# Optimization experiments

Measured on AMD Instinct MI355X. Metric: run time of the kernel, lower is better.

## Reference

```python
import jax, jax.numpy as jnp
import numpy as np
import math

H, D, DEG = 8, 64, 2
GATE_BIAS = 6.906768

def _rope(x, sin, cos):
    # GPT-J style interleaved rotary: even lanes = x1*cos - x2*sin, odd = x2*cos + x1*sin
    x1, x2 = x[..., ::2], x[..., 1::2]
    s = sin[None, :, None, :]
    c = cos[None, :, None, :]
    even = x1 * c - x2 * s
    odd = x2 * c + x1 * s
    return jnp.stack([even, odd], axis=-1).reshape(x.shape)

def _forward(x, w_attn, w_proj):
    B, T, C = x.shape
    h, d, deg = H, D, DEG
    hd = h * d
    scale = 1.0 / math.sqrt(d)
    qkvg = x @ w_attn                                   # (B,T,3hd+h)
    q = qkvg[..., :hd].reshape(B, T, h, d)
    k = qkvg[..., hd:2 * hd].reshape(B, T, h, d)
    v = qkvg[..., 2 * hd:3 * hd].reshape(B, T, h, d)
    log_g = jax.nn.log_sigmoid(GATE_BIAS + qkvg[..., 3 * hd:].astype(jnp.float32))  # (B,T,h)
    # sinusoidal RoPE with frequency 2*pi / T**(2i/d), as in get_sinusoidal_embeddings
    pos = jnp.arange(T, dtype=jnp.float32)
    div = 2.0 * math.pi / (float(T) ** (jnp.arange(0, d, 2, dtype=jnp.float32) / d))
    ang = pos[:, None] * div[None, :]                   # (T, d//2)
    sin, cos = jnp.sin(ang), jnp.cos(ang)
    q = _rope(q, sin, cos)
    k = _rope(k, sin, cos)
    # gated symmetric-power attention: quadratic reference of chunked power_full
    # score_ts = (scale * q_t . k_s)^deg * exp(L_t - L_s), causal, row-normalized
    L = jnp.cumsum(log_g, axis=1).transpose(0, 2, 1)    # (B,h,T) cumulative log-gates
    qk = jnp.einsum('bthd,bshd->bhts', q, k) * scale    # (B,h,T,T)
    log_gate = L[:, :, :, None] - L[:, :, None, :]      # L_t - L_s
    causal = jnp.tril(jnp.ones((T, T), dtype=bool))
    scores = jnp.where(causal, (qk ** deg) * jnp.exp(log_gate), 0.0)
    denom = jnp.maximum(scores.sum(-1, keepdims=True), 1e-6)
    y = jnp.einsum('bhts,bshd->bthd', scores / denom, v)  # (B,T,h,d)
    return y.reshape(B, T, hd) @ w_proj

def setup_inputs() -> dict:
    key = jax.random.key(0)
    k1, k2, k3 = jax.random.split(key, 3)
    B, T, C = 2, 2048, 512
    x = jax.random.normal(k1, (B, T, C), dtype=jnp.float32)
    w_attn = jax.random.normal(k2, (C, 3 * H * D + H), dtype=jnp.float32) * 0.02
    w_proj = jax.random.normal(k3, (H * D, C), dtype=jnp.float32) * 0.02
    return {"x": x, "w_attn": w_attn, "w_proj": w_proj}

def reference(x, w_attn, w_proj):
    return _forward(x, w_attn, w_proj)
```

## Files before the change

### kernel.cpp

```cpp
#include <hip/hip_runtime.h>
#include <hip/hip_bf16.h>
#include <math.h>

constexpr int B_ = 2, T_ = 2048, C_ = 512, H_ = 8, D_ = 64;
constexpr int QKVG_ = 3 * H_ * D_ + H_;
constexpr float GATE_BIAS_ = 6.906768f;
constexpr int N1_ = 1536;
constexpr int SC_ = 8;
constexpr int NBLK_ = 1280;
constexpr int MC_ = 4096 * 512;
constexpr int BHT_ = B_ * H_ * T_;

typedef __attribute__((ext_vector_type(8))) short short8;
typedef __attribute__((ext_vector_type(4))) float f32x4;

__device__ __forceinline__ unsigned short f2b(float f) {
    union { __hip_bfloat16 h; unsigned short u; } cv;
    cv.h = __float2bfloat16(f);
    return cv.u;
}
__device__ __forceinline__ short8 pack8(float4 a, float4 b) {
    short8 r;
    r[0] = (short)f2b(a.x); r[1] = (short)f2b(a.y);
    r[2] = (short)f2b(a.z); r[3] = (short)f2b(a.w);
    r[4] = (short)f2b(b.x); r[5] = (short)f2b(b.y);
    r[6] = (short)f2b(b.z); r[7] = (short)f2b(b.w);
    return r;
}

__device__ __forceinline__ void gl2lds16(const unsigned short* g, void* lds_base) {
    __builtin_amdgcn_global_load_lds(
        (const __attribute__((address_space(1))) unsigned int*)g,
        (__attribute__((address_space(3))) unsigned int*)lds_base, 16, 0, 0);
}

__device__ __forceinline__ void packT_body(
    const float* __restrict__ W, unsigned short* __restrict__ Bt,
    int K, int N, int ldW, int nt, int kt, int tid, float (*Ws)[65])
{
    {
        const int r = tid >> 2;
        const int c0 = (tid & 3) * 16;
#pragma unroll
        for (int j = 0; j < 16; ++j) {
            const int n = nt + c0 + j;
            Ws[r][c0 + j] = (n < N) ? W[(size_t)(kt + r) * ldW + n] : 0.f;
        }
    }
    __syncthreads();
    {
        const int d = tid >> 2;
        const int cc = tid & 3;
        const int kc = cc * 16;
        short8 o0, o1;
#pragma unroll
        for (int j = 0; j < 8; ++j) o0[j] = (short)f2b(Ws[kc + j][d]);
#pragma unroll
        for (int j = 0; j < 8; ++j) o1[j] = (short)f2b(Ws[kc + 8 + j][d]);
        const int row = nt + d;
        unsigned short* op = Bt + (size_t)row * K + kt;
        *(short8*)(op + ((2 * cc) ^ (row & 7)) * 8)     = o0;
        *(short8*)(op + ((2 * cc + 1) ^ (row & 7)) * 8) = o1;
    }
}

__global__ __launch_bounds__(256) void pack_inputs(
    const float* __restrict__ x, const float* __restrict__ w_attn,
    const float* __restrict__ w_proj, unsigned short* __restrict__ xb,
    unsigned short* __restrict__ Bt1, unsigned short* __restrict__ Bt2,
    float2* __restrict__ sincos, float* __restrict__ g)
{
    __shared__ float SM[64 * 65];
    float (*Ws)[65] = (float(*)[65])SM;
    const int bid = blockIdx.x;
    const int tid = threadIdx.x;
    if (bid < 1024) {
        const int i = bid * 256 + tid;
        float4 f0 = *(const float4*)(x + (size_t)i * 8);
        float4 f1 = *(const float4*)(x + (size_t)i * 8 + 4);
        const int row = i >> 6;
        const int ic = i & 63;
        const int swc = (ic & ~7) | ((ic & 7) ^ (row & 7));
        *(short8*)(xb + (size_t)row * 512 + swc * 8) = pack8(f0, f1);
    } else if (bid < 1216) {
        const int q = bid - 1024;
        packT_body(w_attn, Bt1, C_, N1_, QKVG_, (q % 24) * 64, (q / 24) * 64, tid, Ws);
    } else if (bid < 1280) {
        const int q = bid - 1216;
        packT_body(w_proj, Bt2, H_ * D_, C_, C_, (q & 7) * 64, (q >> 3) * 64, tid, Ws);
    } else if (bid < 1288) {
        const int t = (bid - 1280) * 256 + tid;
        float2* op = sincos + (size_t)t * 32;
#pragma unroll
        for (int i = 0; i < 32; ++i) {
            const float div = 6.2831853071795864f * exp2f((float)i * (-11.0f / 32.0f));
            const float ang = (float)t * div;
            op[i] = make_float2(cosf(ang), sinf(ang));
        }
    } else {
        const int q = bid - 1288;
        float* LDSw = SM;
        {
            const int k = tid * 2;
#pragma unroll
            for (int kk = 0; kk < 2; ++kk) {
                const float* wp = w_attn + (size_t)(k + kk) * QKVG_ + 1536;
                float4 wa = *(const float4*)wp;
                float4 wb = *(const float4*)(wp + 4);
                float* dst = LDSw + (k + kk) * 8;
                *(float4*)dst = wa;
                *(float4*)(dst + 4) = wb;
            }
        }
        __syncthreads();
        const int m = q * 32 + (tid >> 3);
        const int h = tid & 7;
        const float* xrow = x + (size_t)m * C_;
        float s = 0.f;
#pragma unroll 4
        for (int k0 = 0; k0 < 512; k0 += 4) {
            float4 xv = *(const float4*)(xrow + k0);
            s += xv.x * LDSw[(k0 + 0) * 8 + h] + xv.y * LDSw[(k0 + 1) * 8 + h]
               + xv.z * LDSw[(k0 + 2) * 8 + h] + xv.w * LDSw[(k0 + 3) * 8 + h];
        }
        const int b = m >> 11, t = m & 2047;
        g[(size_t)(b * 8 + h) * T_ + t] = s;
    }
}

__global__ __launch_bounds__(256) void gate_cumsum(
    const float* __restrict__ g, float* __restrict__ Lg)
{
    __shared__ float wsum[4];
    const int bh = blockIdx.x;
    const int tid = threadIdx.x;
    const int lane = tid & 63, wv = tid >> 6;

    const float* gp = g + (size_t)bh * T_ + tid * 8;
    float v[8];
    float s = 0.f;
#pragma unroll
    for (int j = 0; j < 8; ++j) {
        const float z = gp[j] + GATE_BIAS_;
        const float lg = (z > 0.f) ? -log1pf(expf(-z)) : (z - log1pf(expf(z)));
        s += lg;
        v[j] = s;
    }
    float ssum = s;
#pragma unroll
    for (int off = 1; off < 64; off <<= 1) {
        float n = __shfl_up(ssum, off, 64);
        if (lane >= off) ssum += n;
    }
    if (lane == 63) wsum[wv] = ssum;
    __syncthreads();
    float base = ssum - s;
#pragma unroll
    for (int w = 0; w < 3; ++w)
        base += (w < wv) ? wsum[w] : 0.f;

    float* op = Lg + (size_t)bh * T_ + tid * 8;
#pragma unroll
    for (int j = 0; j < 8; ++j) op[j] = v[j] + base;
}

__global__ __launch_bounds__(256) void gemm_fused(
    const unsigned short* __restrict__ A, const unsigned short* __restrict__ Bt,
    const float* __restrict__ Lg, const float2* __restrict__ sincos,
    unsigned short* __restrict__ Qsb, unsigned short* __restrict__ Ksb,
    unsigned short* __restrict__ Vtb)
{
    __shared__ __align__(16) char smem[65536];
    float (*epi)[65] = (float(*)[65])smem;

    const int tid = threadIdx.x;
    const int wave = tid >> 6, lane = tid & 63;
    const int l15 = lane & 15, lhi = lane >> 4;
    const int wr = wave >> 1, wc = wave & 1;
    const int bm = blockIdx.y * 128, bn = blockIdx.x * 128;

    f32x4 acc[4][4];
#pragma unroll
    for (int i = 0; i < 4; ++i)
#pragma unroll
        for (int j = 0; j < 4; ++j) acc[i][j] = (f32x4){0.f, 0.f, 0.f, 0.f};

    const unsigned short* Arow = A + (size_t)bm * C_;
    const unsigned short* Brow = Bt + (size_t)bn * C_;
    const int sw = (l15 & 7) << 4;
    const int srow = tid >> 3;
    const int schunk = tid & 7;

#pragma unroll
    for (int p = 0; p < 4; ++p) {
        const int row = p * 32 + srow;
        const size_t goff = (size_t)row * C_ + schunk * 8;
        gl2lds16(Arow + goff, smem + p * 4096 + wave * 1024);
        gl2lds16(Brow + goff, smem + 16384 + p * 4096 + wave * 1024);
    }

    for (int ks = 0; ks < 8; ++ks) {
        __syncthreads();
        if (ks < 7) {
            char* dst = smem + ((ks + 1) & 1) * 32768;
            const int k1 = (ks + 1) * 64;
#pragma unroll
            for (int p = 0; p < 4; ++p) {
                const int row = p * 32 + srow;
                const size_t goff = (size_t)row * C_ + k1 + schunk * 8;
                gl2lds16(Arow + goff, dst + p * 4096 + wave * 1024);
                gl2lds16(Brow + goff, dst + 16384 + p * 4096 + wave * 1024);
            }
        }
        const char* AsB = smem + (ks & 1) * 32768;
        const char* BsB = AsB + 16384;

        short8 af[4][2];
#pragma unroll
        for (int mi = 0; mi < 4; ++mi) {
            const int row = wr * 64 + mi * 16 + l15;
#pragma unroll
            for (int kk = 0; kk < 2; ++kk)
                af[mi][kk] = *(const short8*)(AsB + row * 128 + ((kk * 64 + lhi * 16) ^ sw));
        }
#pragma unroll
        for (int ni = 0; ni < 4; ++ni) {
            const int row = wc * 64 + ni * 16 + l15;
            short8 bf0 = *(const short8*)(BsB + row * 128 + ((lhi * 16) ^ sw));
            short8 bf1 = *(const short8*)(BsB + row * 128 + ((64 + lhi * 16) ^ sw));
#pragma unroll
            for (int mi = 0; mi < 4; ++mi) {
                acc[mi][ni] = __builtin_amdgcn_mfma_f32_16x16x32_bf16(af[mi][0], bf0, acc[mi][ni], 0, 0, 0);
                acc[mi][ni] = __builtin_amdgcn_mfma_f32_16x16x32_bf16(af[mi][1], bf1, acc[mi][ni], 0, 0, 0);
            }
        }
    }

    const int rid = bn >> 9;
    const int b = bm >> 11;
    const int tloc0 = bm & 2047;

#pragma unroll
    for (int hc = 0; hc < 2; ++hc) {
        __syncthreads();
        if (wc == hc) {
#pragma unroll
            for (int mi = 0; mi < 4; ++mi)
#pragma unroll
                for (int ni = 0; ni < 4; ++ni)
#pragma unroll
                    for (int r = 0; r < 4; ++r)
                        epi[wr * 64 + mi * 16 + lhi * 4 + r][ni * 16 + l15] = acc[mi][ni][r];
        }
        __syncthreads();
        const int h = ((bn & 511) >> 6) + hc;
        const int bh = b * 8 + h;
        if (rid < 2) {
            const int row = tid >> 1;
            const int c0 = (tid & 1) * 32;
            const int t = tloc0 + row;
            const float Lt = Lg[(size_t)bh * T_ + t];
            const float scl = (rid == 0) ? (__expf(0.5f * Lt) * 0.125f)
                                         : __expf(-0.5f * Lt);
            float vb[32];
#pragma unroll
            for (int j = 0; j < 32; ++j) vb[j] = epi[row][c0 + j];
            const float2* sct = sincos + (size_t)t * 32 + (c0 >> 1);
#pragma unroll
            for (int p = 0; p < 16; ++p) {
                const float2 cssn = sct[p];
                const float x1 = vb[2 * p], x2 = vb[2 * p + 1];
                vb[2 * p]     = (x1 * cssn.x - x2 * cssn.y) * scl;
                vb[2 * p + 1] = (x2 * cssn.x + x1 * cssn.y) * scl;
            }
            unsigned short* op = ((rid == 0) ? Qsb : Ksb) + ((size_t)bh * T_ + t) * 64;
#pragma unroll
            for (int j = 0; j < 4; ++j) {
                short8 o = pack8(*(float4*)&vb[j * 8], *(float4*)&vb[j * 8 + 4]);
                const int chunk = (c0 >> 3) + j;
                const int pos = (rid == 0) ? chunk : (chunk ^ (t & 7));
                *(short8*)(op + pos * 8) = o;
            }
        } else {
            const int d = tid >> 2;
            const int tq = tid & 3;
            unsigned short* op = Vtb + ((size_t)(bh * 64 + d)) * T_;
#pragma unroll
            for (int j = 0; j < 4; ++j) {
                const int tl = tq * 32 + j * 8;
                short8 o;
#pragma unroll
                for (int e = 0; e < 8; ++e)
                    o[e] = (short)f2b(epi[tl + e][d]);
                const int chunkidx = (tloc0 + tl) >> 3;
                const int pos = (chunkidx & ~7) | ((chunkidx & 7) ^ (d & 7));
                *(short8*)(op + pos * 8) = o;
            }
        }
    }
}

__global__ __launch_bounds__(256) void gemm_bf16(
    const unsigned short* __restrict__ A, const unsigned short* __restrict__ Bt,
    float* __restrict__ C, int M, int N, int K)
{
    __shared__ __align__(16) char smem[49152];

    const int tid = threadIdx.x;
    const int wave = tid >> 6, lane = tid & 63;
    const int l15 = lane & 15, lhi = lane >> 4;
    const int wr = wave >> 1, wc = wave & 1;
    const int bm = blockIdx.y * 64, bn = blockIdx.x * 128;

    f32x4 acc[2][4];
#pragma unroll
    for (int i = 0; i < 2; ++i)
#pragma unroll
        for (int j = 0; j < 4; ++j) acc[i][j] = (f32x4){0.f, 0.f, 0.f, 0.f};

    const unsigned short* Arow = A + (size_t)bm * K;
    const unsigned short* Brow = Bt + (size_t)bn * K;
    const int sw = (l15 & 7) << 4;
    const int srow = tid >> 3;
    const int schunk = tid & 7;
    const int nks = K >> 6;

#pragma unroll
    for (int p = 0; p < 2; ++p) {
        const int row = p * 32 + srow;
        gl2lds16(Arow + (size_t)row * K + schunk * 8, smem + p * 4096 + wave * 1024);
    }
#pragma unroll
    for (int p = 0; p < 4; ++p) {
        const int row = p * 32 + srow;
        gl2lds16(Brow + (size_t)row * K + schunk * 8, smem + 8192 + p * 4096 + wave * 1024);
    }

    for (int ks = 0; ks < nks; ++ks) {
        __syncthreads();
        if (ks + 1 < nks) {
            char* dst = smem + ((ks + 1) & 1) * 24576;
            const int k1 = (ks + 1) * 64;
#pragma unroll
            for (int p = 0; p < 2; ++p) {
                const int row = p * 32 + srow;
                gl2lds16(Arow + (size_t)row * K + k1 + schunk * 8, dst + p * 4096 + wave * 1024);
            }
#pragma unroll
            for (int p = 0; p < 4; ++p) {
                const int row = p * 32 + srow;
                gl2lds16(Brow + (size_t)row * K + k1 + schunk * 8, dst + 8192 + p * 4096 + wave * 1024);
            }
        }
        const char* AsB = smem + (ks & 1) * 24576;
        const char* BsB = AsB + 8192;

        short8 af[2][2];
#pragma unroll
        for (int mi = 0; mi < 2; ++mi) {
            const int row = wr * 32 + mi * 16 + l15;
#pragma unroll
            for (int kk = 0; kk < 2; ++kk)
                af[mi][kk] = *(const short8*)(AsB + row * 128 + ((kk * 64 + lhi * 16) ^ sw));
        }
#pragma unroll
        for (int ni = 0; ni < 4; ++ni) {
            const int row = wc * 64 + ni * 16 + l15;
            short8 bf0 = *(const short8*)(BsB + row * 128 + ((lhi * 16) ^ sw));
            short8 bf1 = *(const short8*)(BsB + row * 128 + ((64 + lhi * 16) ^ sw));
#pragma unroll
            for (int mi = 0; mi < 2; ++mi) {
                acc[mi][ni] = __builtin_amdgcn_mfma_f32_16x16x32_bf16(af[mi][0], bf0, acc[mi][ni], 0, 0, 0);
                acc[mi][ni] = __builtin_amdgcn_mfma_f32_16x16x32_bf16(af[mi][1], bf1, acc[mi][ni], 0, 0, 0);
            }
        }
    }

#pragma unroll
    for (int mi = 0; mi < 2; ++mi) {
        const int gm = bm + wr * 32 + mi * 16 + lhi * 4;
#pragma unroll
        for (int r = 0; r < 4; ++r) {
            float* crow = C + (size_t)(gm + r) * N;
#pragma unroll
            for (int ni = 0; ni < 4; ++ni) {
                const int gn = bn + wc * 64 + ni * 16 + l15;
                if (gn < N) crow[gn] = acc[mi][ni][r];
            }
        }
    }
}

__global__ __launch_bounds__(256) void attn_mfma(
    const unsigned short* __restrict__ Qsb, const unsigned short* __restrict__ Ksb,
    const unsigned short* __restrict__ Vtb,
    float* __restrict__ Y0, float* __restrict__ Yp, float* __restrict__ Dpart)
{
    __shared__ __align__(16) char smem[40960];
    char* PsB = smem + 32768;

    const int wg = blockIdx.x;
    const int xcd = wg & 7;
    const int slot = wg >> 3;
    const int bh = (slot < 80) ? xcd : 8 + xcd;
    const int rem = (slot < 80) ? slot : slot - 80;
    const int rr = 79 - rem;
    int bt, sc;
    if (rr < 8)       { bt = rr; sc = 0; }
    else if (rr < 24) { const int q = rr - 8;  bt = 8 + (q >> 1);  sc = q & 1; }
    else if (rr < 48) { const int q = rr - 24; bt = 16 + q / 3;    sc = q % 3; }
    else              { const int q = rr - 48; bt = 24 + (q >> 2); sc = q & 3; }
    const int st0 = sc * SC_;
    const int st1 = min(st0 + SC_ - 1, bt);

    const int tid = threadIdx.x;
    const int wave = tid >> 6;
    const int lane = tid & 63;
    const int l15 = lane & 15;
    const int lhi = lane >> 4;
    const int b = bh >> 3, h = bh & 7;
    const int t0 = bt * 64;

    const int qrow = t0 + wave * 16 + l15;
    const unsigned short* qpp = Qsb + ((size_t)bh * T_ + qrow) * 64 + lhi * 8;
    short8 qf[2];
    qf[0] = *(const short8*)(qpp);
    qf[1] = *(const short8*)(qpp + 32);

    f32x4 accY[4];
#pragma unroll
    for (int n = 0; n < 4; ++n) accY[n] = (f32x4){0.f, 0.f, 0.f, 0.f};
    float den[4] = {0.f, 0.f, 0.f, 0.f};

    const int kchunk = lhi * 16;
    const int rsw = (l15 & 7) << 4;
    const int srow = tid >> 3;
    const int schunk = tid & 7;

#pragma unroll
    for (int p = 0; p < 2; ++p) {
        const int row = p * 32 + srow;
        gl2lds16(Ksb + ((size_t)bh * T_ + st0 * 64 + row) * 64 + schunk * 8,
                 smem + p * 4096 + wave * 1024);
        gl2lds16(Vtb + ((size_t)bh * 64 + row) * T_ + st0 * 64 + schunk * 8,
                 smem + 8192 + p * 4096 + wave * 1024);
    }

    for (int st = st0; st <= st1; ++st) {
        __syncthreads();
        if (st < st1) {
            char* dst = smem + (((st - st0) + 1) & 1) * 16384;
            const int s1 = (st + 1) * 64;
#pragma unroll
            for (int p = 0; p < 2; ++p) {
                const int row = p * 32 + srow;
                gl2lds16(Ksb + ((size_t)bh * T_ + s1 + row) * 64 + schunk * 8,
                         dst + p * 4096 + wave * 1024);
                gl2lds16(Vtb + ((size_t)bh * 64 + row) * T_ + s1 + schunk * 8,
                         dst + 8192 + p * 4096 + wave * 1024);
            }
        }
        const char* KsB = smem + ((st - st0) & 1) * 16384;
        const char* VtB = KsB + 8192;

        f32x4 accS[4];
#pragma unroll
        for (int n = 0; n < 4; ++n) accS[n] = (f32x4){0.f, 0.f, 0.f, 0.f};
        __builtin_amdgcn_s_setprio(1);
#pragma unroll
        for (int n = 0; n < 4; ++n) {
#pragma unroll
            for (int kk = 0; kk < 2; ++kk) {
                short8 bf = *(const short8*)(KsB + (n * 16 + l15) * 128 + ((kk * 64 + kchunk) ^ rsw));
                accS[n] = __builtin_amdgcn_mfma_f32_16x16x32_bf16(qf[kk], bf, accS[n], 0, 0, 0);
            }
        }
        __builtin_amdgcn_s_setprio(0);

        const bool last = (st == bt);
        char* PsW = PsB + wave * 2048;
#pragma unroll
        for (int n = 0; n < 4; ++n) {
#pragma unroll
            for (int r = 0; r < 4; ++r) {
                const float a = accS[n][r];
                float p = a * a;
                if (last)
                    p = ((n * 16 + l15) <= wave * 16 + lhi * 4 + r) ? p : 0.f;
                den[r] += p;
                const int prow = lhi * 4 + r;
                *(unsigned short*)(PsW + prow * 128 + ((2 * (n * 16 + l15)) ^ ((prow & 7) << 4))) = f2b(p);
            }
        }

        short8 pa[2];
#pragma unroll
        for (int kk = 0; kk < 2; ++kk)
            pa[kk] = *(const short8*)(PsW + l15 * 128 + ((kk * 64 + kchunk) ^ rsw));
        __builtin_amdgcn_s_setprio(1);
#pragma unroll
        for (int n = 0; n < 4; ++n) {
#pragma unroll
            for (int kk = 0; kk < 2; ++kk) {
                short8 vb = *(const short8*)(VtB + (n * 16 + l15) * 128 + ((kk * 64 + kchunk) ^ rsw));
                accY[n] = __builtin_amdgcn_mfma_f32_16x16x32_bf16(pa[kk], vb, accY[n], 0, 0, 0);
            }
        }
        __builtin_amdgcn_s_setprio(0);
    }

#pragma unroll
    for (int r = 0; r < 4; ++r) {
        den[r] += __shfl_xor(den[r], 1, 64);
        den[r] += __shfl_xor(den[r], 2, 64);
        den[r] += __shfl_xor(den[r], 4, 64);
        den[r] += __shfl_xor(den[r], 8, 64);
    }

    float* Ybase = (sc == 0) ? Y0 : (Yp + (size_t)(sc - 1) * MC_);
    float* Dbase = Dpart + (size_t)sc * BHT_;
#pragma unroll
    for (int r = 0; r < 4; ++r) {
        const int t = t0 + wave * 16 + lhi * 4 + r;
        if (l15 == 0)
            Dbase[(size_t)bh * T_ + t] = den[r];
        float* yo = Ybase + (size_t)(b * T_ + t) * (H_ * D_) + h * 64 + l15;
#pragma unroll
        for (int n = 0; n < 4; ++n)
            yo[n * 16] = accY[n][r];
    }
}

__global__ __launch_bounds__(256) void normalize_kernel(
    const float* __restrict__ Y0, const float* __restrict__ Yp,
    const float* __restrict__ Dpart, unsigned short* __restrict__ ybb)
{
    const int gid = blockIdx.x * 256 + threadIdx.x;
    const size_t base = (size_t)gid * 8;
    const int row = (int)(base >> 9);
    const int col = (int)(base & 511);
    const int b = row >> 11, t = row & 2047, h = col >> 6;
    const int bh = b * H_ + h;
    const int nsc = ((t >> 6) >> 3) + 1;

    float d = Dpart[(size_t)bh * T_ + t];
    float4 f0 = *(const float4*)(Y0 + base);
    float4 f1 = *(const float4*)(Y0 + base + 4);
    for (int s = 1; s < nsc; ++s) {
        d += Dpart[(size_t)s * BHT_ + (size_t)bh * T_ + t];
        const float* yp = Yp + (size_t)(s - 1) * MC_ + base;
        float4 g0 = *(const float4*)(yp);
        float4 g1 = *(const float4*)(yp + 4);
        f0.x += g0.x; f0.y += g0.y; f0.z += g0.z; f0.w += g0.w;
        f1.x += g1.x; f1.y += g1.y; f1.z += g1.z; f1.w += g1.w;
    }
    const float inv = 1.0f / fmaxf(d, 1e-6f);
    f0.x *= inv; f0.y *= inv; f0.z *= inv; f0.w *= inv;
    f1.x *= inv; f1.y *= inv; f1.z *= inv; f1.w *= inv;

    const int ic = col >> 3;
    const int swc = (ic & ~7) | ((ic & 7) ^ (row & 7));
    *(short8*)(ybb + (size_t)row * 512 + swc * 8) = pack8(f0, f1);
}

extern "C" void kernel_launch(void* const* d_in, const int* in_sizes, int n_in,
                              void* d_out, int out_size, void* d_ws, size_t ws_size,
                              hipStream_t stream)
{
    const float* x      = (const float*)d_in[0];
    const float* w_attn = (const float*)d_in[1];
    const float* w_proj = (const float*)d_in[2];
    float* out = (float*)d_out;

    char* p = (char*)d_ws;
    float2* sincos = (float2*)p;               p += (size_t)T_ * 32 * 8;
    float* g       = (float*)p;                p += (size_t)BHT_ * 4;
    float* Lg      = (float*)p;                p += (size_t)BHT_ * 4;
    float* Dpart   = (float*)p;                p += (size_t)4 * BHT_ * 4;
    unsigned short* xb  = (unsigned short*)p;  p += (size_t)MC_ * 2;
    unsigned short* Bt1 = (unsigned short*)p;  p += (size_t)N1_ * C_ * 2;
    unsigned short* Bt2 = (unsigned short*)p;  p += (size_t)C_ * C_ * 2;
    unsigned short* Qsb = (unsigned short*)p;  p += (size_t)BHT_ * 64 * 2;
    unsigned short* Ksb = (unsigned short*)p;  p += (size_t)BHT_ * 64 * 2;
    unsigned short* Vtb = (unsigned short*)p;  p += (size_t)BHT_ * 64 * 2;
    float* Yp      = (float*)p;                p += (size_t)3 * MC_ * 4;
    unsigned short* ybb = (unsigned short*)p;

    const int M = B_ * T_;

    pack_inputs<<<1416, 256, 0, stream>>>(x, w_attn, w_proj, xb, Bt1, Bt2, sincos, g);

    gate_cumsum<<<B_ * H_, 256, 0, stream>>>(g, Lg);

    gemm_fused<<<dim3(N1_ / 128, M / 128), 256, 0, stream>>>(
        xb, Bt1, Lg, sincos, Qsb, Ksb, Vtb);

    attn_mfma<<<NBLK_, 256, 0, stream>>>(Qsb, Ksb, Vtb, out, Yp, Dpart);

    normalize_kernel<<<(MC_ / 8) / 256, 256, 0, stream>>>(out, Yp, Dpart, ybb);

    gemm_bf16<<<dim3(C_ / 128, M / 64), 256, 0, stream>>>(
        ybb, Bt2, out, M, C_, H_ * D_);
}
```

Baseline: 79.15 us.

## Enlarge attention query tile to 128 rows to reuse K/V tiles across two row-tiles

```diff
diff --git a/kernel.cpp b/kernel.cpp
--- a/kernel.cpp
+++ b/kernel.cpp
@@ -6,8 +6,7 @@
 constexpr int QKVG_ = 3 * H_ * D_ + H_;
 constexpr float GATE_BIAS_ = 6.906768f;
 constexpr int N1_ = 1536;
-constexpr int SC_ = 8;
-constexpr int NBLK_ = 1280;
+constexpr int NBLK_ = 640;
 constexpr int MC_ = 4096 * 512;
 constexpr int BHT_ = B_ * H_ * T_;
 
@@ -396,22 +395,22 @@
     const unsigned short* __restrict__ Vtb,
     float* __restrict__ Y0, float* __restrict__ Yp, float* __restrict__ Dpart)
 {
-    __shared__ __align__(16) char smem[40960];
+    __shared__ __align__(16) char smem[49152];
     char* PsB = smem + 32768;
 
     const int wg = blockIdx.x;
     const int xcd = wg & 7;
     const int slot = wg >> 3;
-    const int bh = (slot < 80) ? xcd : 8 + xcd;
-    const int rem = (slot < 80) ? slot : slot - 80;
-    const int rr = 79 - rem;
-    int bt, sc;
-    if (rr < 8)       { bt = rr; sc = 0; }
-    else if (rr < 24) { const int q = rr - 8;  bt = 8 + (q >> 1);  sc = q & 1; }
-    else if (rr < 48) { const int q = rr - 24; bt = 16 + q / 3;    sc = q % 3; }
-    else              { const int q = rr - 48; bt = 24 + (q >> 2); sc = q & 3; }
-    const int st0 = sc * SC_;
-    const int st1 = min(st0 + SC_ - 1, bt);
+    const int bh = (slot < 40) ? xcd : 8 + xcd;
+    const int rem = (slot < 40) ? slot : slot - 40;
+    const int rr = 39 - rem;
+    int btq, sc;
+    if (rr < 4)       { btq = rr; sc = 0; }
+    else if (rr < 12) { const int q = rr - 4;  btq = 4 + (q >> 1);  sc = q & 1; }
+    else if (rr < 24) { const int q = rr - 12; btq = 8 + q / 3;     sc = q % 3; }
+    else              { const int q = rr - 24; btq = 12 + (q >> 2); sc = q & 3; }
+    const int st0 = sc * 8;
+    const int st1 = min(st0 + 7, 2 * btq + 1);
 
     const int tid = threadIdx.x;
     const int wave = tid >> 6;
@@ -419,18 +418,23 @@
     const int l15 = lane & 15;
     const int lhi = lane >> 4;
     const int b = bh >> 3, h = bh & 7;
-    const int t0 = bt * 64;
-
-    const int qrow = t0 + wave * 16 + l15;
-    const unsigned short* qpp = Qsb + ((size_t)bh * T_ + qrow) * 64 + lhi * 8;
-    short8 qf[2];
-    qf[0] = *(const short8*)(qpp);
-    qf[1] = *(const short8*)(qpp + 32);
-
-    f32x4 accY[4];
-#pragma unroll
-    for (int n = 0; n < 4; ++n) accY[n] = (f32x4){0.f, 0.f, 0.f, 0.f};
-    float den[4] = {0.f, 0.f, 0.f, 0.f};
+    const int t0 = btq * 128;
+
+    short8 qf[2][2];
+#pragma unroll
+    for (int rt = 0; rt < 2; ++rt) {
+        const int qrow = t0 + wave * 32 + rt * 16 + l15;
+        const unsigned short* qpp = Qsb + ((size_t)bh * T_ + qrow) * 64 + lhi * 8;
+        qf[rt][0] = *(const short8*)(qpp);
+        qf[rt][1] = *(const short8*)(qpp + 32);
+    }
+
+    f32x4 accY[2][4];
+#pragma unroll
+    for (int rt = 0; rt < 2; ++rt)
+#pragma unroll
+        for (int n = 0; n < 4; ++n) accY[rt][n] = (f32x4){0.f, 0.f, 0.f, 0.f};
+    float den[2][4] = {{0.f, 0.f, 0.f, 0.f}, {0.f, 0.f, 0.f, 0.f}};
 
     const int kchunk = lhi * 16;
     const int rsw = (l15 & 7) << 4;
@@ -463,71 +467,90 @@
         const char* KsB = smem + ((st - st0) & 1) * 16384;
         const char* VtB = KsB + 8192;
 
-        f32x4 accS[4];
-#pragma unroll
-        for (int n = 0; n < 4; ++n) accS[n] = (f32x4){0.f, 0.f, 0.f, 0.f};
+        f32x4 accS[2][4];
+#pragma unroll
+        for (int rt = 0; rt < 2; ++rt)
+#pragma unroll
+            for (int n = 0; n < 4; ++n) accS[rt][n] = (f32x4){0.f, 0.f, 0.f, 0.f};
         __builtin_amdgcn_s_setprio(1);
 #pragma unroll
         for (int n = 0; n < 4; ++n) {
 #pragma unroll
             for (int kk = 0; kk < 2; ++kk) {
                 short8 bf = *(const short8*)(KsB + (n * 16 + l15) * 128 + ((kk * 64 + kchunk) ^ rsw));
-                accS[n] = __builtin_amdgcn_mfma_f32_16x16x32_bf16(qf[kk], bf, accS[n], 0, 0, 0);
+#pragma unroll
+                for (int rt = 0; rt < 2; ++rt)
+                    accS[rt][n] = __builtin_amdgcn_mfma_f32_16x16x32_bf16(qf[rt][kk], bf, accS[rt][n], 0, 0, 0);
             }
         }
         __builtin_amdgcn_s_setprio(0);
 
-        const bool last = (st == bt);
-        char* PsW = PsB + wave * 2048;
-#pragma unroll
-        for (int n = 0; n < 4; ++n) {
-#pragma unroll
-            for (int r = 0; r < 4; ++r) {
-                const float a = accS[n][r];
-                float p = a * a;
-                if (last)
-                    p = ((n * 16 + l15) <= wave * 16 + lhi * 4 + r) ? p : 0.f;
-                den[r] += p;
-                const int prow = lhi * 4 + r;
-                *(unsigned short*)(PsW + prow * 128 + ((2 * (n * 16 + l15)) ^ ((prow & 7) << 4))) = f2b(p);
-            }
-        }
-
-        short8 pa[2];
-#pragma unroll
-        for (int kk = 0; kk < 2; ++kk)
-            pa[kk] = *(const short8*)(PsW + l15 * 128 + ((kk * 64 + kchunk) ^ rsw));
+        const bool msk = (st >= 2 * btq);
+        char* PsW = PsB + wave * 4096;
+#pragma unroll
+        for (int rt = 0; rt < 2; ++rt) {
+#pragma unroll
+            for (int n = 0; n < 4; ++n) {
+#pragma unroll
+                for (int r = 0; r < 4; ++r) {
+                    const float a = accS[rt][n][r];
+                    float p = a * a;
+                    if (msk) {
+                        const int scol = st * 64 + n * 16 + l15;
+                        const int trow = t0 + wave * 32 + rt * 16 + lhi * 4 + r;
+                        p = (scol <= trow) ? p : 0.f;
+                    }
+                    den[rt][r] += p;
+                    const int prow = rt * 16 + lhi * 4 + r;
+                    *(unsigned short*)(PsW + prow * 128 + ((2 * (n * 16 + l15)) ^ ((prow & 7) << 4))) = f2b(p);
+                }
+            }
+        }
+
+        short8 pa[2][2];
+#pragma unroll
+        for (int rt = 0; rt < 2; ++rt)
+#pragma unroll
+            for (int kk = 0; kk < 2; ++kk)
+                pa[rt][kk] = *(const short8*)(PsW + (rt * 16 + l15) * 128 + ((kk * 64 + kchunk) ^ rsw));
         __builtin_amdgcn_s_setprio(1);
 #pragma unroll
         for (int n = 0; n < 4; ++n) {
 #pragma unroll
             for (int kk = 0; kk < 2; ++kk) {
                 short8 vb = *(const short8*)(VtB + (n * 16 + l15) * 128 + ((kk * 64 + kchunk) ^ rsw));
-                accY[n] = __builtin_amdgcn_mfma_f32_16x16x32_bf16(pa[kk], vb, accY[n], 0, 0, 0);
+#pragma unroll
+                for (int rt = 0; rt < 2; ++rt)
+                    accY[rt][n] = __builtin_amdgcn_mfma_f32_16x16x32_bf16(pa[rt][kk], vb, accY[rt][n], 0, 0, 0);
             }
         }
         __builtin_amdgcn_s_setprio(0);
     }
 
 #pragma unroll
-    for (int r = 0; r < 4; ++r) {
-        den[r] += __shfl_xor(den[r], 1, 64);
-        den[r] += __shfl_xor(den[r], 2, 64);
-        den[r] += __shfl_xor(den[r], 4, 64);
-        den[r] += __shfl_xor(den[r], 8, 64);
-    }
+    for (int rt = 0; rt < 2; ++rt)
+#pragma unroll
+        for (int r = 0; r < 4; ++r) {
+            den[rt][r] += __shfl_xor(den[rt][r], 1, 64);
+            den[rt][r] += __shfl_xor(den[rt][r], 2, 64);
+            den[rt][r] += __shfl_xor(den[rt][r], 4, 64);
+            den[rt][r] += __shfl_xor(den[rt][r], 8, 64);
+        }
 
     float* Ybase = (sc == 0) ? Y0 : (Yp + (size_t)(sc - 1) * MC_);
     float* Dbase = Dpart + (size_t)sc * BHT_;
 #pragma unroll
-    for (int r = 0; r < 4; ++r) {
-        const int t = t0 + wave * 16 + lhi * 4 + r;
-        if (l15 == 0)
-            Dbase[(size_t)bh * T_ + t] = den[r];
-        float* yo = Ybase + (size_t)(b * T_ + t) * (H_ * D_) + h * 64 + l15;
-#pragma unroll
-        for (int n = 0; n < 4; ++n)
-            yo[n * 16] = accY[n][r];
+    for (int rt = 0; rt < 2; ++rt) {
+#pragma unroll
+        for (int r = 0; r < 4; ++r) {
+            const int t = t0 + wave * 32 + rt * 16 + lhi * 4 + r;
+            if (l15 == 0)
+                Dbase[(size_t)bh * T_ + t] = den[rt][r];
+            float* yo = Ybase + (size_t)(b * T_ + t) * (H_ * D_) + h * 64 + l15;
+#pragma unroll
+            for (int n = 0; n < 4; ++n)
+                yo[n * 16] = accY[rt][n][r];
+        }
     }
 }
 
@@ -541,7 +564,7 @@
     const int col = (int)(base & 511);
     const int b = row >> 11, t = row & 2047, h = col >> 6;
     const int bh = b * H_ + h;
-    const int nsc = ((t >> 6) >> 3) + 1;
+    const int nsc = (t >> 9) + 1;
 
     float d = Dpart[(size_t)bh * T_ + t];
     float4 f0 = *(const float4*)(Y0 + base);
```

Result: slower. 82.22 us (+3.9%).

## Double attention query tile to 128 rows with 512-thread blocks sharing K/V tiles

Applied to the files above, without the earlier changes.

```diff
diff --git a/kernel.cpp b/kernel.cpp
--- a/kernel.cpp
+++ b/kernel.cpp
@@ -6,8 +6,7 @@
 constexpr int QKVG_ = 3 * H_ * D_ + H_;
 constexpr float GATE_BIAS_ = 6.906768f;
 constexpr int N1_ = 1536;
-constexpr int SC_ = 8;
-constexpr int NBLK_ = 1280;
+constexpr int NBLK_ = 640;
 constexpr int MC_ = 4096 * 512;
 constexpr int BHT_ = B_ * H_ * T_;
 
@@ -391,27 +390,27 @@
     }
 }
 
-__global__ __launch_bounds__(256) void attn_mfma(
+__global__ __launch_bounds__(512) void attn_mfma(
     const unsigned short* __restrict__ Qsb, const unsigned short* __restrict__ Ksb,
     const unsigned short* __restrict__ Vtb,
     float* __restrict__ Y0, float* __restrict__ Yp, float* __restrict__ Dpart)
 {
-    __shared__ __align__(16) char smem[40960];
+    __shared__ __align__(16) char smem[49152];
     char* PsB = smem + 32768;
 
     const int wg = blockIdx.x;
     const int xcd = wg & 7;
     const int slot = wg >> 3;
-    const int bh = (slot < 80) ? xcd : 8 + xcd;
-    const int rem = (slot < 80) ? slot : slot - 80;
-    const int rr = 79 - rem;
-    int bt, sc;
-    if (rr < 8)       { bt = rr; sc = 0; }
-    else if (rr < 24) { const int q = rr - 8;  bt = 8 + (q >> 1);  sc = q & 1; }
-    else if (rr < 48) { const int q = rr - 24; bt = 16 + q / 3;    sc = q % 3; }
-    else              { const int q = rr - 48; bt = 24 + (q >> 2); sc = q & 3; }
-    const int st0 = sc * SC_;
-    const int st1 = min(st0 + SC_ - 1, bt);
+    const int bh = (slot < 40) ? xcd : 8 + xcd;
+    const int rem = (slot < 40) ? slot : slot - 40;
+    const int rr = 39 - rem;
+    int btq, sc;
+    if (rr < 4)       { btq = rr; sc = 0; }
+    else if (rr < 12) { const int q = rr - 4;  btq = 4 + (q >> 1);  sc = q & 1; }
+    else if (rr < 24) { const int q = rr - 12; btq = 8 + q / 3;     sc = q % 3; }
+    else              { const int q = rr - 24; btq = 12 + (q >> 2); sc = q & 3; }
+    const int st0 = sc * 8;
+    const int st1 = min(st0 + 7, 2 * btq + 1);
 
     const int tid = threadIdx.x;
     const int wave = tid >> 6;
@@ -419,7 +418,7 @@
     const int l15 = lane & 15;
     const int lhi = lane >> 4;
     const int b = bh >> 3, h = bh & 7;
-    const int t0 = bt * 64;
+    const int t0 = btq * 128;
 
     const int qrow = t0 + wave * 16 + l15;
     const unsigned short* qpp = Qsb + ((size_t)bh * T_ + qrow) * 64 + lhi * 8;
@@ -437,28 +436,20 @@
     const int srow = tid >> 3;
     const int schunk = tid & 7;
 
-#pragma unroll
-    for (int p = 0; p < 2; ++p) {
-        const int row = p * 32 + srow;
-        gl2lds16(Ksb + ((size_t)bh * T_ + st0 * 64 + row) * 64 + schunk * 8,
-                 smem + p * 4096 + wave * 1024);
-        gl2lds16(Vtb + ((size_t)bh * 64 + row) * T_ + st0 * 64 + schunk * 8,
-                 smem + 8192 + p * 4096 + wave * 1024);
-    }
+    gl2lds16(Ksb + ((size_t)bh * T_ + st0 * 64 + srow) * 64 + schunk * 8,
+             smem + wave * 1024);
+    gl2lds16(Vtb + ((size_t)bh * 64 + srow) * T_ + st0 * 64 + schunk * 8,
+             smem + 8192 + wave * 1024);
 
     for (int st = st0; st <= st1; ++st) {
         __syncthreads();
         if (st < st1) {
             char* dst = smem + (((st - st0) + 1) & 1) * 16384;
             const int s1 = (st + 1) * 64;
-#pragma unroll
-            for (int p = 0; p < 2; ++p) {
-                const int row = p * 32 + srow;
-                gl2lds16(Ksb + ((size_t)bh * T_ + s1 + row) * 64 + schunk * 8,
-                         dst + p * 4096 + wave * 1024);
-                gl2lds16(Vtb + ((size_t)bh * 64 + row) * T_ + s1 + schunk * 8,
-                         dst + 8192 + p * 4096 + wave * 1024);
-            }
+            gl2lds16(Ksb + ((size_t)bh * T_ + s1 + srow) * 64 + schunk * 8,
+                     dst + wave * 1024);
+            gl2lds16(Vtb + ((size_t)bh * 64 + srow) * T_ + s1 + schunk * 8,
+                     dst + 8192 + wave * 1024);
         }
         const char* KsB = smem + ((st - st0) & 1) * 16384;
         const char* VtB = KsB + 8192;
@@ -477,7 +468,7 @@
         }
         __builtin_amdgcn_s_setprio(0);
 
-        const bool last = (st == bt);
+        const bool msk = (st >= 2 * btq);
         char* PsW = PsB + wave * 2048;
 #pragma unroll
         for (int n = 0; n < 4; ++n) {
@@ -485,8 +476,11 @@
             for (int r = 0; r < 4; ++r) {
                 const float a = accS[n][r];
                 float p = a * a;
-                if (last)
-                    p = ((n * 16 + l15) <= wave * 16 + lhi * 4 + r) ? p : 0.f;
+                if (msk) {
+                    const int scol = st * 64 + n * 16 + l15;
+                    const int trow = t0 + wave * 16 + lhi * 4 + r;
+                    p = (scol <= trow) ? p : 0.f;
+                }
                 den[r] += p;
                 const int prow = lhi * 4 + r;
                 *(unsigned short*)(PsW + prow * 128 + ((2 * (n * 16 + l15)) ^ ((prow & 7) << 4))) = f2b(p);
@@ -541,7 +535,7 @@
     const int col = (int)(base & 511);
     const int b = row >> 11, t = row & 2047, h = col >> 6;
     const int bh = b * H_ + h;
-    const int nsc = ((t >> 6) >> 3) + 1;
+    const int nsc = (t >> 9) + 1;
 
     float d = Dpart[(size_t)bh * T_ + t];
     float4 f0 = *(const float4*)(Y0 + base);
@@ -595,7 +589,7 @@
     gemm_fused<<<dim3(N1_ / 128, M / 128), 256, 0, stream>>>(
         xb, Bt1, Lg, sincos, Qsb, Ksb, Vtb);
 
-    attn_mfma<<<NBLK_, 256, 0, stream>>>(Qsb, Ksb, Vtb, out, Yp, Dpart);
+    attn_mfma<<<NBLK_, 512, 0, stream>>>(Qsb, Ksb, Vtb, out, Yp, Dpart);
 
     normalize_kernel<<<(MC_ / 8) / 256, 256, 0, stream>>>(out, Yp, Dpart, ybb);
 
```

Result: no change. 80.08 us (+1.2%).
